# Optimization experiments

Measured on AMD Instinct MI355X. Metric: run time of the kernel, lower is better.

## Reference

```python
import jax, jax.numpy as jnp
import numpy as np

D = 128          # kg_emb_dim
H = 8            # mha_n_heads
N = 20000        # sub-graph nodes per modality
NNZ = 500000     # incidence entries per modality
E = 5000         # hyperedges per modality
C = 50           # context entities
NENT = 50000     # n_entity (rec vocab)


def hyperconv(x, theta, bias, nodes, edges, num_edges):
    # PyG-style HypergraphConv: out = D^-1 H B^-1 H^T (X Theta) + b
    xt = x @ theta                                             # [N, D]
    ones = jnp.ones(nodes.shape[0], xt.dtype)
    e_sum = jax.ops.segment_sum(xt[nodes], edges, num_segments=num_edges)   # [E, D]
    e_deg = jax.ops.segment_sum(ones, edges, num_segments=num_edges)        # [E]
    m = e_sum / jnp.maximum(e_deg, 1.0)[:, None]               # hyperedge means
    n_sum = jax.ops.segment_sum(m[edges], nodes, num_segments=x.shape[0])   # [N, D]
    n_deg = jax.ops.segment_sum(ones, nodes, num_segments=x.shape[0])       # [N]
    return n_sum / jnp.maximum(n_deg, 1.0)[:, None] + bias


def mha(q_x, kv_x, Wq, bq, Wk, bk, Wv, bv, Wo, bo):
    # torch.nn.MultiheadAttention math, batch of 1 (squeezed)
    dh = D // H
    q = (q_x @ Wq + bq).reshape(-1, H, dh)
    k = (kv_x @ Wk + bk).reshape(-1, H, dh)
    v = (kv_x @ Wv + bv).reshape(-1, H, dh)
    scores = jnp.einsum('qhd,khd->hqk', q, k) / jnp.sqrt(jnp.asarray(dh, q.dtype))
    attn = jax.nn.softmax(scores, axis=-1)
    out = jnp.einsum('hqk,khd->qhd', attn, v).reshape(-1, D)
    return out @ Wo + bo


def self_attn(h, a, b):
    # SelfAttentionBatch: softmax(tanh(h a) b) weighted sum over rows
    e = (jnp.tanh(h @ a) @ b)[:, 0]
    return jax.nn.softmax(e) @ h


def setup_inputs() -> dict:
    ks = jax.random.split(jax.random.key(0), 32)
    s = D ** (-0.5)
    inp = {
        'item_emb':   jax.random.normal(ks[0], (N, D), jnp.float32) * s,
        'entity_emb': jax.random.normal(ks[1], (N, D), jnp.float32) * s,
        'word_emb':   jax.random.normal(ks[2], (N, D), jnp.float32) * s,
        'context_entity': jax.random.normal(ks[3], (C, D), jnp.float32) * s,
        'theta_item':   jax.random.normal(ks[4], (D, D), jnp.float32) * s,
        'bias_item':    jax.random.normal(ks[5], (D,), jnp.float32) * 0.02,
        'theta_entity': jax.random.normal(ks[6], (D, D), jnp.float32) * s,
        'bias_entity':  jax.random.normal(ks[7], (D,), jnp.float32) * 0.02,
        'theta_word':   jax.random.normal(ks[8], (D, D), jnp.float32) * s,
        'bias_word':    jax.random.normal(ks[9], (D,), jnp.float32) * 0.02,
        'Wq': jax.random.normal(ks[10], (D, D), jnp.float32) * s,
        'bq': jax.random.normal(ks[11], (D,), jnp.float32) * 0.02,
        'Wk': jax.random.normal(ks[12], (D, D), jnp.float32) * s,
        'bk': jax.random.normal(ks[13], (D,), jnp.float32) * 0.02,
        'Wv': jax.random.normal(ks[14], (D, D), jnp.float32) * s,
        'bv': jax.random.normal(ks[15], (D,), jnp.float32) * 0.02,
        'Wo': jax.random.normal(ks[16], (D, D), jnp.float32) * s,
        'bo': jax.random.normal(ks[17], (D,), jnp.float32) * 0.02,
        'a_his': jax.random.normal(ks[18], (D, D), jnp.float32) * s,
        'b_his': jax.random.normal(ks[19], (D, 1), jnp.float32) * s,
        'a_kg':  jax.random.normal(ks[20], (D, D), jnp.float32) * s,
        'b_kg':  jax.random.normal(ks[21], (D, 1), jnp.float32) * s,
        'rec_W': jax.random.normal(ks[22], (D, NENT), jnp.float32) * s,
        'rec_b': jax.random.normal(ks[23], (NENT,), jnp.float32) * 0.02,
        'item_nodes':   jax.random.randint(ks[24], (NNZ,), 0, N, jnp.int32),
        'item_edges':   jax.random.randint(ks[25], (NNZ,), 0, E, jnp.int32),
        'entity_nodes': jax.random.randint(ks[26], (NNZ,), 0, N, jnp.int32),
        'entity_edges': jax.random.randint(ks[27], (NNZ,), 0, E, jnp.int32),
        'word_nodes':   jax.random.randint(ks[28], (NNZ,), 0, N, jnp.int32),
        'word_edges':   jax.random.randint(ks[29], (NNZ,), 0, E, jnp.int32),
    }
    return inp


def reference(item_emb, entity_emb, word_emb, context_entity,
              theta_item, bias_item, theta_entity, bias_entity, theta_word, bias_word,
              Wq, bq, Wk, bk, Wv, bv, Wo, bo,
              a_his, b_his, a_kg, b_kg, rec_W, rec_b,
              item_nodes, item_edges, entity_nodes, entity_edges, word_nodes, word_edges):
    ih = hyperconv(item_emb, theta_item, bias_item, item_nodes, item_edges, E)
    eh = hyperconv(entity_emb, theta_entity, bias_entity, entity_nodes, entity_edges, E)
    wh = hyperconv(word_emb, theta_word, bias_word, word_nodes, word_edges, E)
    related = jnp.concatenate([ih, eh, wh], axis=0)            # [3N, D]
    # MHItemAttention: context queries attend over related embeddings
    attentive = mha(context_entity, related, Wq, bq, Wk, bk, Wv, bv, Wo, bo)  # [C, D]
    u = self_attn(attentive, a_his, b_his)                     # [D]
    user = jnp.concatenate([context_entity, u[None]], axis=0)  # [C+1, D]
    user_repr = self_attn(user, a_kg, b_kg)                    # [D]
    scores = user_repr @ rec_W + rec_b                         # [NENT]
    return scores
```

## Files before the change

### kernel.cpp

```cpp
#include <hip/hip_runtime.h>
#include <hip/hip_bf16.h>

#define D_ 128
#define H_ 8
#define N_ 20000
#define NNZ_ 500000
#define E_ 5000
#define C_ 50
#define NENT_ 50000
#define NK_ (3*N_)
#define CAPE_ 192
#define CAPN_ 64
#define ENT_PB 4096
#define NBKT 157
#define BCAP 3648
#define ABLK 123
#define NCH3 118
#define KVBLK 235

struct Ptr3f { const float* p[3]; };
struct Ptr3i { const int* p[3]; };
struct GemmB { const float* A[3]; const float* W[3]; unsigned short* C[3]; };

typedef short bf16x8 __attribute__((ext_vector_type(8)));
typedef float f32x4  __attribute__((ext_vector_type(4)));

__device__ __forceinline__ unsigned short f2b(float f){
  unsigned u = __float_as_uint(f);
  u += 0x7FFFu + ((u>>16)&1u);
  return (unsigned short)(u>>16);
}
__device__ __forceinline__ unsigned pk2(float a, float b){
  return (unsigned)f2b(a) | ((unsigned)f2b(b) << 16);
}
__device__ __forceinline__ float blo(unsigned u){ return __uint_as_float(u<<16); }
__device__ __forceinline__ float bhi(unsigned u){ return __uint_as_float(u & 0xFFFF0000u); }

#define PB_PACK 7500
#define PB_Z    7628
#define PB_Q    7629
#define PB_CTX  7693
#define PB_TOT  7743
__global__ __launch_bounds__(256) void prep(Ptr3f xs, unsigned short* __restrict__ xb,
    const float* __restrict__ Wk, const float* __restrict__ Wv, unsigned short* __restrict__ bfB,
    int* __restrict__ gcnt_e, int* __restrict__ gcnt_n,
    const float* __restrict__ ctx, const float* __restrict__ Wq, const float* __restrict__ bq,
    unsigned short* __restrict__ bfQ,
    const float* __restrict__ a2, const float* __restrict__ b2, float* __restrict__ e2)
{
  int bid = blockIdx.x, t = threadIdx.x;
  if (bid < PB_PACK){
    int mod = bid / 2500, blk = bid - mod*2500;
    int i4 = blk*256 + t;
    float4 v = *(const float4*)(xs.p[mod] + (size_t)i4*4);
    ushort4 o; o.x=f2b(v.x); o.y=f2b(v.y); o.z=f2b(v.z); o.w=f2b(v.w);
    *(ushort4*)(xb + (size_t)mod*N_*D_ + (size_t)i4*4) = o;
  } else if (bid < PB_Z){
    int idx = (bid - PB_PACK)*256 + t;
    int j  = idx & 7;
    int L  = (idx >> 3) & 63;
    int kb = (idx >> 9) & 3;
    int tt = idx >> 11;
    int k = kb*32 + (L>>4)*8 + j;
    int x = L & 15;
    float v = (tt < 8) ? Wk[(size_t)k*128 + tt*16 + x] : Wv[(size_t)k*128 + (tt-8)*16 + x];
    bfB[idx] = f2b(v);
  } else if (bid == PB_Z){
    for (int i=t; i<3*NBKT; i+=256){ gcnt_e[i]=0; gcnt_n[i]=0; }
  } else if (bid < PB_CTX){
    int idx = (bid - PB_Q)*256 + t;
    int j  = idx & 7;
    int L  = (idx >> 3) & 63;
    int qt = (idx >> 9) & 3;
    int h  = idx >> 11;
    int k  = ((L>>4)&3)*8 + j;
    int q  = qt*16 + (L & 15);
    float val = 0.f;
    if (k < 16 && q < C_){
      const float* cr = ctx + (size_t)q*128;
      const float* wc = Wq + h*16 + k;
      float s0=0.f,s1=0.f,s2=0.f,s3=0.f;
      for (int d=0; d<128; d+=4){
        s0 = fmaf(cr[d],   wc[(size_t) d   *128], s0);
        s1 = fmaf(cr[d+1], wc[(size_t)(d+1)*128], s1);
        s2 = fmaf(cr[d+2], wc[(size_t)(d+2)*128], s2);
        s3 = fmaf(cr[d+3], wc[(size_t)(d+3)*128], s3);
      }
      val = 0.25f * (s0+s1+s2+s3 + bq[h*16+k]);
    }
    bfQ[idx] = f2b(val);
  } else {
    __shared__ float row[128];
    __shared__ float ps[128][2];
    __shared__ float red[2];
    int q = bid - PB_CTX;
    if (t < 128) row[t] = ctx[(size_t)q*128 + t];
    __syncthreads();
    int c = t & 127, half = t >> 7;
    float s = 0.f;
    int d0 = half*64;
    for (int d=d0; d<d0+64; d+=4){
      s = fmaf(row[d],   a2[(size_t) d   *128 + c], s);
      s = fmaf(row[d+1], a2[(size_t)(d+1)*128 + c], s);
      s = fmaf(row[d+2], a2[(size_t)(d+2)*128 + c], s);
      s = fmaf(row[d+3], a2[(size_t)(d+3)*128 + c], s);
    }
    ps[c][half] = s;
    __syncthreads();
    if (t < 128){
      float v = tanhf(ps[t][0] + ps[t][1]) * b2[t];
      #pragma unroll
      for (int k=32; k>=1; k>>=1) v += __shfl_xor(v, k);
      if ((t & 63) == 0) red[t>>6] = v;
    }
    __syncthreads();
    if (t == 0) e2[q] = red[0] + red[1];
  }
}

__global__ __launch_bounds__(256) void binA(Ptr3i nodes, Ptr3i edges,
    unsigned* __restrict__ pe_part, unsigned* __restrict__ pn_part,
    int* __restrict__ gcnt_e, int* __restrict__ gcnt_n)
{
  __shared__ unsigned lbin[ENT_PB];
  __shared__ int cnt[256], off[256];
  __shared__ int gbase[NBKT];
  __shared__ int wsum[4];
  const int mod = blockIdx.y;
  const int* nd = nodes.p[mod];
  const int* ed = edges.p[mod];
  const int base = blockIdx.x * ENT_PB;
  const int t = threadIdx.x;
  const int lane = t & 63, w = t >> 6;

  int myn[16], mye[16], pos[16];
  #pragma unroll
  for (int k=0;k<16;k++){
    int i = base + t + k*256;
    if (i < NNZ_){ myn[k]=nd[i]; mye[k]=ed[i]; }
    else { myn[k]=-1; mye[k]=-1; }
  }

  cnt[t] = 0;
  __syncthreads();
  #pragma unroll
  for (int k=0;k<16;k++)
    if (mye[k] >= 0) pos[k] = atomicAdd(&cnt[mye[k]>>5], 1);
  __syncthreads();
  {
    int v = cnt[t], s = v;
    #pragma unroll
    for (int d=1; d<64; d<<=1){ int u=__shfl_up(s,d); if (lane>=d) s+=u; }
    if (lane==63) wsum[w]=s;
    __syncthreads();
    int wb=0;
    for (int i=0;i<w;i++) wb+=wsum[i];
    off[t] = wb + s - v;
    __syncthreads();
  }
  #pragma unroll
  for (int k=0;k<16;k++)
    if (mye[k] >= 0)
      lbin[off[mye[k]>>5] + pos[k]] = ((unsigned)mye[k] << 15) | (unsigned)myn[k];
  if (t < NBKT && cnt[t] > 0) gbase[t] = atomicAdd(&gcnt_e[mod*NBKT + t], cnt[t]);
  __syncthreads();
  {
    int total = off[255];
    unsigned* dstreg = pe_part + (size_t)mod*NBKT*BCAP;
    for (int i=t; i<total; i+=256){
      unsigned pk = lbin[i];
      int b = pk >> 20;
      int gp = gbase[b] + (i - off[b]);
      if (gp < BCAP) dstreg[(size_t)b*BCAP + gp] = pk;
    }
  }
  __syncthreads();

  cnt[t] = 0;
  __syncthreads();
  #pragma unroll
  for (int k=0;k<16;k++)
    if (myn[k] >= 0) pos[k] = atomicAdd(&cnt[myn[k]>>7], 1);
  __syncthreads();
  {
    int v = cnt[t], s = v;
    #pragma unroll
    for (int d=1; d<64; d<<=1){ int u=__shfl_up(s,d); if (lane>=d) s+=u; }
    if (lane==63) wsum[w]=s;
    __syncthreads();
    int wb=0;
    for (int i=0;i<w;i++) wb+=wsum[i];
    off[t] = wb + s - v;
    __syncthreads();
  }
  #pragma unroll
  for (int k=0;k<16;k++)
    if (myn[k] >= 0)
      lbin[off[myn[k]>>7] + pos[k]] = ((unsigned)myn[k] << 13) | (unsigned)mye[k];
  if (t < NBKT && cnt[t] > 0) gbase[t] = atomicAdd(&gcnt_n[mod*NBKT + t], cnt[t]);
  __syncthreads();
  {
    int total = off[255];
    unsigned* dstreg = pn_part + (size_t)mod*NBKT*BCAP;
    for (int i=t; i<total; i+=256){
      unsigned pk = lbin[i];
      int b = pk >> 20;
      int gp = gbase[b] + (i - off[b]);
      if (gp < BCAP) dstreg[(size_t)b*BCAP + gp] = pk;
    }
  }
}

__global__ __launch_bounds__(256) void binB(const unsigned* __restrict__ pe_part,
    const unsigned* __restrict__ pn_part,
    const int* __restrict__ gcnt_e, const int* __restrict__ gcnt_n,
    int* __restrict__ cnt_all, int* __restrict__ cntA_e,
    unsigned short* __restrict__ e_slot, unsigned short* __restrict__ n_slot)
{
  __shared__ unsigned short ls[128*CAPN_];
  __shared__ int lc[128];
  const int y = blockIdx.y, b = blockIdx.x, t = threadIdx.x;
  if (y < 3){
    const int mod = y;
    if (t < 64) lc[t] = 0;
    __syncthreads();
    int cnt = gcnt_e[mod*NBKT + b];
    if (cnt > BCAP) cnt = BCAP;
    const unsigned* src = pe_part + ((size_t)mod*NBKT + b)*BCAP;
    for (int i=t; i<cnt; i+=256){
      unsigned pk = src[i];
      int el = (pk >> 15) - b*32;
      int n  = pk & 0x7FFF;
      if (n < (N_>>1)){
        int p = atomicAdd(&lc[el], 1);
        if (p < 96) ls[el*CAPE_ + p] = (unsigned short)n;
      } else {
        int p = atomicAdd(&lc[32 + el], 1);
        if (p < 96) ls[el*CAPE_ + (CAPE_-1 - p)] = (unsigned short)n;
      }
    }
    __syncthreads();
    int rows = E_ - b*32; if (rows > 32) rows = 32;
    if (t < rows){
      cnt_all[mod*(E_+N_) + b*32 + t] = lc[t] + lc[32+t];
      cntA_e[mod*E_ + b*32 + t] = lc[t];
    }
    const unsigned* lsu = (const unsigned*)ls;
    unsigned* dst = (unsigned*)(e_slot + ((size_t)mod*E_ + b*32)*CAPE_);
    int tot = rows*CAPE_/2;
    for (int i=t; i<tot; i+=256) dst[i] = lsu[i];
  } else {
    const int mod = y - 3;
    if (t < 128) lc[t] = 0;
    __syncthreads();
    int cnt = gcnt_n[mod*NBKT + b];
    if (cnt > BCAP) cnt = BCAP;
    const unsigned* src = pn_part + ((size_t)mod*NBKT + b)*BCAP;
    for (int i=t; i<cnt; i+=256){
      unsigned pk = src[i];
      int nl = (pk >> 13) - b*128;
      int e  = pk & 0x1FFF;
      int p = atomicAdd(&lc[nl], 1);
      if (p < CAPN_) ls[nl*CAPN_ + p] = (unsigned short)e;
    }
    __syncthreads();
    int rows = N_ - b*128; if (rows > 128) rows = 128;
    if (t < rows) cnt_all[mod*(E_+N_) + E_ + b*128 + t] = lc[t];
    const unsigned* lsu = (const unsigned*)ls;
    unsigned* dst = (unsigned*)(n_slot + ((size_t)mod*N_ + b*128)*CAPN_);
    int tot = rows*CAPN_/2;
    for (int i=t; i<tot; i+=256) dst[i] = lsu[i];
  }
}

#define EGB 3752
template<int PHASE>
__global__ __launch_bounds__(256) void e_gather_ph(const unsigned short* __restrict__ xb,
    const int* __restrict__ cnt_all, const int* __restrict__ cntA_e,
    const unsigned short* __restrict__ e_slot, float* __restrict__ m_mean)
{
  const int bid = blockIdx.x;
  const int x = bid & 7, k = bid >> 3;
  int mod, r;
  if (x < 6){
    mod = x / 3;
    int li = x - mod*3;
    int c = 417 - (li == 2);
    if (k < c){
      r = k*3 + li;
    } else {
      int hg = 52*x + (x >= 3) + (k - c);
      mod = 2; r = 938 + hg;
      if (r >= E_/4) return;
    }
  } else {
    mod = 2; r = k*2 + (x - 6);
  }
  const int w = threadIdx.x >> 6, lane = threadIdx.x & 63;
  const int rgrp = lane >> 4, dl = lane & 15;
  const int e = r*4 + w;
  const unsigned short* xt = xb + (size_t)mod*N_*D_;
  int cnt = cnt_all[mod*(E_+N_) + e];
  int cAr = cntA_e[mod*E_ + e];
  int cA = (cAr < 96) ? cAr : 96;
  int cBr = cnt - cAr;
  int cB = (cBr < 96) ? cBr : 96;
  const unsigned short* slot = e_slot + ((size_t)mod*E_ + e)*CAPE_;
  float a0=0.f,a1=0.f,a2=0.f,a3=0.f,a4=0.f,a5=0.f,a6=0.f,a7=0.f;

  if (PHASE == 0){
    int sv0 = slot[lane], sv1 = slot[64 + lane];
    for (int j=0; j<cA; j+=32){
      uint4 uu[8];
      #pragma unroll
      for (int kk=0;kk<8;kk++){
        int jr = j + 4*kk + rgrp;
        int jj = (jr < cA) ? jr : 0;
        int i0 = __shfl(sv0, jj & 63);
        int i1 = __shfl(sv1, jj & 63);
        int idx = (jj < 64) ? i0 : i1;
        uu[kk] = *(const uint4*)(xt + (size_t)idx*128 + dl*8);
      }
      #pragma unroll
      for (int kk=0;kk<8;kk++){
        int jr = j + 4*kk + rgrp;
        bool v = jr < cA;
        unsigned x0 = v ? uu[kk].x : 0u, x1 = v ? uu[kk].y : 0u;
        unsigned x2 = v ? uu[kk].z : 0u, x3 = v ? uu[kk].w : 0u;
        a0 += blo(x0); a1 += bhi(x0); a2 += blo(x1); a3 += bhi(x1);
        a4 += blo(x2); a5 += bhi(x2); a6 += blo(x3); a7 += bhi(x3);
      }
    }
  } else {
    int sv1 = slot[64 + lane], sv2 = slot[128 + lane];
    int s0 = CAPE_ - cB;
    for (int j=0; j<cB; j+=32){
      uint4 uu[8];
      #pragma unroll
      for (int kk=0;kk<8;kk++){
        int jr = j + 4*kk + rgrp;
        int jj = (jr < cB) ? (s0 + jr) : (CAPE_-1);
        int i1 = __shfl(sv1, jj & 63);
        int i2 = __shfl(sv2, jj & 63);
        int idx = (jj < 128) ? i1 : i2;
        uu[kk] = *(const uint4*)(xt + (size_t)idx*128 + dl*8);
      }
      #pragma unroll
      for (int kk=0;kk<8;kk++){
        int jr = j + 4*kk + rgrp;
        bool v = jr < cB;
        unsigned x0 = v ? uu[kk].x : 0u, x1 = v ? uu[kk].y : 0u;
        unsigned x2 = v ? uu[kk].z : 0u, x3 = v ? uu[kk].w : 0u;
        a0 += blo(x0); a1 += bhi(x0); a2 += blo(x1); a3 += bhi(x1);
        a4 += blo(x2); a5 += bhi(x2); a6 += blo(x3); a7 += bhi(x3);
      }
    }
  }

  #pragma unroll
  for (int s=16; s<=32; s<<=1){
    a0 += __shfl_xor(a0, s); a1 += __shfl_xor(a1, s);
    a2 += __shfl_xor(a2, s); a3 += __shfl_xor(a3, s);
    a4 += __shfl_xor(a4, s); a5 += __shfl_xor(a5, s);
    a6 += __shfl_xor(a6, s); a7 += __shfl_xor(a7, s);
  }
  if (rgrp == 0){
    float* dst = m_mean + ((size_t)mod*E_ + e)*128 + dl*8;
    if (PHASE == 0){
      float4 o1; o1.x=a0; o1.y=a1; o1.z=a2; o1.w=a3;
      float4 o2; o2.x=a4; o2.y=a5; o2.z=a6; o2.w=a7;
      *(float4*)dst = o1;
      *(float4*)(dst + 4) = o2;
    } else {
      float inv = 1.f / fmaxf((float)cnt, 1.f);
      float4 o1 = *(const float4*)dst;
      float4 o2 = *(const float4*)(dst + 4);
      o1.x = (o1.x + a0)*inv; o1.y = (o1.y + a1)*inv;
      o1.z = (o1.z + a2)*inv; o1.w = (o1.w + a3)*inv;
      o2.x = (o2.x + a4)*inv; o2.y = (o2.y + a5)*inv;
      o2.z = (o2.z + a6)*inv; o2.w = (o2.w + a7)*inv;
      *(float4*)dst = o1;
      *(float4*)(dst + 4) = o2;
    }
  }
}

__global__ __launch_bounds__(256) void gemm_b(GemmB g, int M)
{
  const float* A = g.A[blockIdx.y];
  const float* W = g.W[blockIdx.y];
  unsigned short* Cout = g.C[blockIdx.y];
  __shared__ float As[64][33];
  __shared__ float Ws[32][128];
  const int t  = threadIdx.x;
  const int br = blockIdx.x * 64;
  const int r0 = (t >> 5) * 8;
  const int c0 = (t & 31) * 4;
  const int lr = t >> 2;
  const int lk = (t & 3) * 8;
  const int wk = t >> 5;

  float acc[8][4];
  #pragma unroll
  for (int i=0;i<8;i++){ acc[i][0]=0.f; acc[i][1]=0.f; acc[i][2]=0.f; acc[i][3]=0.f; }

  for (int kb=0; kb<128; kb+=32){
    float av[8];
    const int grow = br + lr;
    if (grow < M){
      const float* p = A + (size_t)grow*128 + kb + lk;
      float4 a = ((const float4*)p)[0], b = ((const float4*)p)[1];
      av[0]=a.x;av[1]=a.y;av[2]=a.z;av[3]=a.w;av[4]=b.x;av[5]=b.y;av[6]=b.z;av[7]=b.w;
    } else {
      #pragma unroll
      for (int j=0;j<8;j++) av[j]=0.f;
    }
    float4 wv4[4];
    #pragma unroll
    for (int kk=0;kk<4;kk++) wv4[kk] = *(const float4*)&W[(size_t)(kb + wk + kk*8)*128 + c0];

    __syncthreads();
    #pragma unroll
    for (int j=0;j<8;j++) As[lr][lk+j] = av[j];
    #pragma unroll
    for (int kk=0;kk<4;kk++) *(float4*)&Ws[wk + kk*8][c0] = wv4[kk];
    __syncthreads();

    #pragma unroll
    for (int k=0;k<32;k++){
      float4 wv = *(const float4*)&Ws[k][c0];
      #pragma unroll
      for (int i=0;i<8;i++){
        float a = As[r0+i][k];
        acc[i][0] = fmaf(a, wv.x, acc[i][0]);
        acc[i][1] = fmaf(a, wv.y, acc[i][1]);
        acc[i][2] = fmaf(a, wv.z, acc[i][2]);
        acc[i][3] = fmaf(a, wv.w, acc[i][3]);
      }
    }
  }

  #pragma unroll
  for (int i=0;i<8;i++){
    int gr = br + r0 + i;
    if (gr < M){
      ushort4 o;
      o.x=f2b(acc[i][0]); o.y=f2b(acc[i][1]); o.z=f2b(acc[i][2]); o.w=f2b(acc[i][3]);
      *(ushort4*)(Cout + (size_t)gr*128 + c0) = o;
    }
  }
}

__global__ __launch_bounds__(256) void n_gather_w(const unsigned short* __restrict__ m_buf,
    const int* __restrict__ cnt_all, const unsigned short* __restrict__ n_slot,
    Ptr3f biases, unsigned short* __restrict__ relbf)
{
  int mod = blockIdx.y;
  int w = threadIdx.x >> 6, lane = threadIdx.x & 63;
  int rgrp = lane >> 4, dl = lane & 15;
  int n = blockIdx.x*4 + w;
  const unsigned short* m = m_buf + (size_t)mod*E_*D_;
  int cnt = cnt_all[mod*(E_+N_) + E_ + n];
  int c2 = (cnt < CAPN_) ? cnt : CAPN_;
  const unsigned short* slot = n_slot + ((size_t)mod*N_ + n)*CAPN_;
  int sv = slot[lane];
  float a0=0.f,a1=0.f,a2=0.f,a3=0.f,a4=0.f,a5=0.f,a6=0.f,a7=0.f;
  for (int j=0; j<c2; j+=32){
    uint4 uu[8];
    #pragma unroll
    for (int k=0;k<8;k++){
      int jr = j + 4*k + rgrp;
      int jj = (jr < c2) ? jr : 0;
      int idx = __shfl(sv, jj);
      uu[k] = *(const uint4*)(m + (size_t)idx*128 + dl*8);
    }
    #pragma unroll
    for (int k=0;k<8;k++){
      int jr = j + 4*k + rgrp;
      bool v = jr < c2;
      unsigned x0 = v ? uu[k].x : 0u, x1 = v ? uu[k].y : 0u;
      unsigned x2 = v ? uu[k].z : 0u, x3 = v ? uu[k].w : 0u;
      a0 += blo(x0); a1 += bhi(x0); a2 += blo(x1); a3 += bhi(x1);
      a4 += blo(x2); a5 += bhi(x2); a6 += blo(x3); a7 += bhi(x3);
    }
  }
  #pragma unroll
  for (int s=16; s<=32; s<<=1){
    a0 += __shfl_xor(a0, s); a1 += __shfl_xor(a1, s);
    a2 += __shfl_xor(a2, s); a3 += __shfl_xor(a3, s);
    a4 += __shfl_xor(a4, s); a5 += __shfl_xor(a5, s);
    a6 += __shfl_xor(a6, s); a7 += __shfl_xor(a7, s);
  }
  if (rgrp == 0){
    float inv = 1.f / fmaxf((float)cnt, 1.f);
    const float* bs = biases.p[mod] + dl*8;
    uint4 o;
    o.x = pk2(a0*inv + bs[0], a1*inv + bs[1]);
    o.y = pk2(a2*inv + bs[2], a3*inv + bs[3]);
    o.z = pk2(a4*inv + bs[4], a5*inv + bs[5]);
    o.w = pk2(a6*inv + bs[6], a7*inv + bs[7]);
    *(uint4*)(relbf + ((size_t)mod*N_ + n)*128 + dl*8) = o;
  }
}

__global__ __launch_bounds__(256) void gemm_kv_mfma(const unsigned short* __restrict__ relbf,
    const unsigned short* __restrict__ bfB, const float* __restrict__ bk,
    const float* __restrict__ bv, unsigned short* __restrict__ Kb,
    unsigned short* __restrict__ Vtg)
{
  __shared__ unsigned short Bs[32768];
  const int t = threadIdx.x, w = t >> 6, L = t & 63;
  const int m = L & 15, quad = L >> 4, x = m;

  {
    const uint4* src = (const uint4*)bfB;
    uint4* dst = (uint4*)Bs;
    for (int i = t; i < 4096; i += 256) dst[i] = src[i];
  }
  __syncthreads();

  const int rowbase = blockIdx.x*256;
  for (int g = 0; g < 4; g++){
    const int j0 = rowbase + g*64 + w*16;

    bf16x8 a[4];
    {
      int row = j0 + m;
      int rowc = (row < NK_) ? row : (NK_-1);
      #pragma unroll
      for (int kb=0; kb<4; kb++)
        a[kb] = *(const bf16x8*)(relbf + (size_t)rowc*128 + kb*32 + quad*8);
    }

    f32x4 acc[16];
    #pragma unroll
    for (int tt=0; tt<16; tt++) acc[tt] = (f32x4){0.f,0.f,0.f,0.f};

    #pragma unroll
    for (int kb=0; kb<4; kb++){
      #pragma unroll
      for (int tt=0; tt<16; tt++){
        bf16x8 b = *(const bf16x8*)&Bs[(((tt*4 + kb)*64 + L) << 3)];
        acc[tt] = __builtin_amdgcn_mfma_f32_16x16x32_bf16(a[kb], b, acc[tt], 0, 0, 0);
      }
    }

    #pragma unroll
    for (int tt=0; tt<16; tt++){
      int h = tt & 7, kv = tt >> 3;
      float bias = (kv ? bv : bk)[h*16 + x];
      #pragma unroll
      for (int r=0; r<4; r++){
        int jr = j0 + quad*4 + r;
        if (jr < NK_){
          unsigned short val = f2b(acc[tt][r] + bias);
          if (kv == 0) Kb[(((size_t)h*NK_ + jr) << 4) + x] = val;
          else         Vtg[((size_t)(h*16 + x))*NK_ + jr] = val;
        }
      }
    }
  }
}

__global__ __launch_bounds__(256) void flash3(const unsigned short* __restrict__ Kb,
    const unsigned short* __restrict__ Vtg, const unsigned short* __restrict__ bfQ,
    float* __restrict__ part)
{
  __shared__ unsigned short P_lds[4][64][40];
  __shared__ float mbuf[4][64][18];
  const int c = blockIdx.x, h = blockIdx.y;
  const int t = threadIdx.x, w = t >> 6, L = t & 63;
  const int n = L & 15, quad = L >> 4;

  bf16x8 qb[4];
  #pragma unroll
  for (int qt=0; qt<4; qt++)
    qb[qt] = *(const bf16x8*)(bfQ + (((h*4 + qt)*64 + L) << 3));

  float Mc[4], Lc[4];
  f32x4 accq[4];
  #pragma unroll
  for (int qt=0; qt<4; qt++){ Mc[qt] = -INFINITY; Lc[qt] = 0.f; accq[qt] = (f32x4){0.f,0.f,0.f,0.f}; }

  const int base = c*512 + w*128;
  unsigned* Pw = (unsigned*)&P_lds[w][0][0];

  for (int tile=0; tile<4; tile++){
    const int j0 = base + tile*32;
    const bool dead = (j0 >= NK_);

    bf16x8 a0 = (bf16x8){0,0,0,0,0,0,0,0};
    bf16x8 a1 = a0;
    if (quad < 2){
      int k0 = j0 + n;      if (k0 > NK_-1) k0 = NK_-1;
      int k1 = j0 + 16 + n; if (k1 > NK_-1) k1 = NK_-1;
      a0 = *(const bf16x8*)(Kb + (((size_t)h*NK_ + k0) << 4) + quad*8);
      a1 = *(const bf16x8*)(Kb + (((size_t)h*NK_ + k1) << 4) + quad*8);
    }
    f32x4 s0[4], s1[4];
    #pragma unroll
    for (int qt=0; qt<4; qt++){
      s0[qt] = __builtin_amdgcn_mfma_f32_16x16x32_bf16(a0, qb[qt], (f32x4){0.f,0.f,0.f,0.f}, 0,0,0);
      s1[qt] = __builtin_amdgcn_mfma_f32_16x16x32_bf16(a1, qb[qt], (f32x4){0.f,0.f,0.f,0.f}, 0,0,0);
    }

    #pragma unroll
    for (int qt=0; qt<4; qt++){
      float mt = s0[qt][0];
      mt = fmaxf(mt, s0[qt][1]); mt = fmaxf(mt, s0[qt][2]); mt = fmaxf(mt, s0[qt][3]);
      mt = fmaxf(mt, s1[qt][0]); mt = fmaxf(mt, s1[qt][1]);
      mt = fmaxf(mt, s1[qt][2]); mt = fmaxf(mt, s1[qt][3]);
      mt = fmaxf(mt, __shfl_xor(mt, 16));
      mt = fmaxf(mt, __shfl_xor(mt, 32));
      float Mn = fmaxf(Mc[qt], mt);
      float corr = __expf(Mc[qt] - Mn);
      Mc[qt] = Mn;
      float p0[4], p1[4];
      #pragma unroll
      for (int r=0;r<4;r++){
        p0[r] = __expf(s0[qt][r] - Mn);
        p1[r] = __expf(s1[qt][r] - Mn);
      }
      if (dead){
        #pragma unroll
        for (int r=0;r<4;r++){ p0[r]=0.f; p1[r]=0.f; }
      }
      float lt = p0[0]+p0[1]+p0[2]+p0[3]+p1[0]+p1[1]+p1[2]+p1[3];
      lt += __shfl_xor(lt, 16);
      lt += __shfl_xor(lt, 32);
      Lc[qt] = Lc[qt]*corr + lt;
      int rb = (qt*16 + n)*20;
      Pw[rb + quad*2]     = pk2(p0[0], p0[1]);
      Pw[rb + quad*2 + 1] = pk2(p0[2], p0[3]);
      Pw[rb + 8 + quad*2]     = pk2(p1[0], p1[1]);
      Pw[rb + 8 + quad*2 + 1] = pk2(p1[2], p1[3]);
      #pragma unroll
      for (int r=0;r<4;r++){
        float cr = __shfl(corr, quad*4 + r);
        accq[qt][r] *= cr;
      }
    }
    __syncthreads();

    bf16x8 bv_;
    {
      int va = j0 + quad*8; if (va > NK_-8) va = NK_-8;
      bv_ = *(const bf16x8*)(Vtg + ((size_t)(h*16 + n))*NK_ + va);
    }
    #pragma unroll
    for (int qt=0; qt<4; qt++){
      bf16x8 pa = *(const bf16x8*)&P_lds[w][qt*16 + n][quad*8];
      accq[qt] = __builtin_amdgcn_mfma_f32_16x16x32_bf16(pa, bv_, accq[qt], 0,0,0);
    }
    __syncthreads();
  }

  #pragma unroll
  for (int qt=0; qt<4; qt++){
    #pragma unroll
    for (int r=0; r<4; r++)
      mbuf[w][qt*16 + quad*4 + r][2 + n] = accq[qt][r];
    if (quad == 0){
      mbuf[w][qt*16 + n][0] = Mc[qt];
      mbuf[w][qt*16 + n][1] = Lc[qt];
    }
  }
  __syncthreads();
  if (t < C_){
    float M = mbuf[0][t][0], Lm = mbuf[0][t][1];
    float A[16];
    #pragma unroll
    for (int i=0;i<16;i++) A[i] = mbuf[0][t][2+i];
    #pragma unroll
    for (int ww=1; ww<4; ww++){
      float pm = mbuf[ww][t][0], pl = mbuf[ww][t][1];
      if (pl > 0.f){
        float mn = fmaxf(M, pm);
        float c1 = __expf(M - mn), c2 = __expf(pm - mn);
        Lm = Lm*c1 + pl*c2;
        #pragma unroll
        for (int i=0;i<16;i++) A[i] = A[i]*c1 + mbuf[ww][t][2+i]*c2;
        M = mn;
      }
    }
    float* pp = part + ((size_t)(h*NCH3 + c)*C_ + t)*18;
    pp[0] = M; pp[1] = Lm;
    #pragma unroll
    for (int i=0;i<16;i++) pp[2+i] = A[i];
  }
}

__global__ __launch_bounds__(512) void merge_oproj_e1(const float* __restrict__ part,
    const float* __restrict__ Wo, const float* __restrict__ bo,
    const float* __restrict__ a1, const float* __restrict__ b1,
    float* __restrict__ attentive, float* __restrict__ e1)
{
  __shared__ float row[128];
  __shared__ float ps[128][4];
  __shared__ float orow[128];
  __shared__ float red[2];
  const int q = blockIdx.x, t = threadIdx.x;
  const int h = t >> 6, lane = t & 63;

  {
    float M = -1e30f, L = 0.f;
    float A[16];
    #pragma unroll
    for (int i=0;i<16;i++) A[i] = 0.f;

    #pragma unroll
    for (int cc=0; cc<2; cc++){
      int c = lane + cc*64;
      if (c < NCH3){
        const float* p = part + ((size_t)(h*NCH3 + c)*C_ + q)*18;
        float pm = p[0], pl = p[1];
        if (pl > 0.f){
          float Mn = fmaxf(M, pm);
          float w1 = __expf(M - Mn), w2 = __expf(pm - Mn);
          L = L*w1 + pl*w2;
          #pragma unroll
          for (int i=0;i<16;i++) A[i] = fmaf(A[i], w1, p[2+i]*w2);
          M = Mn;
        }
      }
    }
    #pragma unroll
    for (int d=32; d>=1; d>>=1){
      float pm = __shfl_xor(M, d);
      float pl = __shfl_xor(L, d);
      float Ao[16];
      #pragma unroll
      for (int i=0;i<16;i++) Ao[i] = __shfl_xor(A[i], d);
      float Mn = fmaxf(M, pm);
      float w1 = __expf(M - Mn), w2 = __expf(pm - Mn);
      L = L*w1 + pl*w2;
      #pragma unroll
      for (int i=0;i<16;i++) A[i] = fmaf(A[i], w1, Ao[i]*w2);
      M = Mn;
    }
    if (lane == 0){
      float invL = 1.f / L;
      #pragma unroll
      for (int i=0;i<16;i++) row[h*16 + i] = A[i]*invL;
    }
  }
  __syncthreads();

  const int c = t & 127, seg = t >> 7;
  {
    float s = 0.f;
    int d0 = seg*32;
    for (int d=d0; d<d0+32; d+=4){
      s = fmaf(row[d],   Wo[(size_t) d   *128 + c], s);
      s = fmaf(row[d+1], Wo[(size_t)(d+1)*128 + c], s);
      s = fmaf(row[d+2], Wo[(size_t)(d+2)*128 + c], s);
      s = fmaf(row[d+3], Wo[(size_t)(d+3)*128 + c], s);
    }
    ps[c][seg] = s;
  }
  __syncthreads();
  if (t < 128){
    float o = ps[t][0]+ps[t][1]+ps[t][2]+ps[t][3] + bo[t];
    attentive[(size_t)q*128 + t] = o;
    orow[t] = o;
  }
  __syncthreads();
  {
    float s = 0.f;
    int d0 = seg*32;
    for (int d=d0; d<d0+32; d+=4){
      s = fmaf(orow[d],   a1[(size_t) d   *128 + c], s);
      s = fmaf(orow[d+1], a1[(size_t)(d+1)*128 + c], s);
      s = fmaf(orow[d+2], a1[(size_t)(d+2)*128 + c], s);
      s = fmaf(orow[d+3], a1[(size_t)(d+3)*128 + c], s);
    }
    ps[c][seg] = s;
  }
  __syncthreads();
  if (t < 128){
    float v = tanhf(ps[t][0]+ps[t][1]+ps[t][2]+ps[t][3]) * b1[t];
    #pragma unroll
    for (int k=32; k>=1; k>>=1) v += __shfl_xor(v, k);
    if ((t & 63) == 0) red[t>>6] = v;
  }
  __syncthreads();
  if (t == 0) e1[q] = red[0] + red[1];
}

__global__ __launch_bounds__(128) void tail_mid(const float* __restrict__ attentive,
    const float* __restrict__ ctx, const float* __restrict__ a2, const float* __restrict__ b2,
    const float* __restrict__ e1, const float* __restrict__ e2, float* __restrict__ user_repr)
{
  __shared__ float p[64];
  __shared__ float u[128];
  __shared__ float red[2];
  __shared__ float p2[64];
  const int t = threadIdx.x;

  if (t == 0){
    float mx=-INFINITY;
    for (int i=0;i<C_;i++) mx=fmaxf(mx,e1[i]);
    float ss=0.f;
    for (int i=0;i<C_;i++){ p[i]=__expf(e1[i]-mx); ss+=p[i]; }
    float inv=1.f/ss;
    for (int i=0;i<C_;i++) p[i]*=inv;
  }
  __syncthreads();
  {
    float s=0.f;
    for (int r=0;r<C_;r++) s = fmaf(p[r], attentive[(size_t)r*128 + t], s);
    u[t] = s;
  }
  __syncthreads();
  {
    float s0=0.f,s1=0.f,s2=0.f,s3=0.f;
    for (int d=0; d<128; d+=4){
      s0 = fmaf(u[d],   a2[(size_t) d   *128 + t], s0);
      s1 = fmaf(u[d+1], a2[(size_t)(d+1)*128 + t], s1);
      s2 = fmaf(u[d+2], a2[(size_t)(d+2)*128 + t], s2);
      s3 = fmaf(u[d+3], a2[(size_t)(d+3)*128 + t], s3);
    }
    float v = tanhf(s0+s1+s2+s3) * b2[t];
    #pragma unroll
    for (int k=32; k>=1; k>>=1) v += __shfl_xor(v, k);
    if ((t & 63) == 0) red[t>>6] = v;
  }
  __syncthreads();
  if (t == 0){
    float elast = red[0] + red[1];
    float mx=elast;
    for (int i=0;i<C_;i++) mx=fmaxf(mx,e2[i]);
    float ss=0.f;
    for (int i=0;i<C_;i++){ p2[i]=__expf(e2[i]-mx); ss+=p2[i]; }
    float pl = __expf(elast-mx); ss += pl;
    float inv=1.f/ss;
    for (int i=0;i<C_;i++) p2[i]*=inv;
    p2[C_] = pl*inv;
  }
  __syncthreads();
  {
    float s=0.f;
    for (int r=0;r<C_;r++) s = fmaf(p2[r], ctx[(size_t)r*128 + t], s);
    s = fmaf(p2[C_], u[t], s);
    user_repr[t] = s;
  }
}

__global__ __launch_bounds__(256) void scores_k(const float* __restrict__ ur,
    const float* __restrict__ recW, const float* __restrict__ recb, float* __restrict__ out)
{
  __shared__ float u[128];
  int t = threadIdx.x;
  if (t < 128) u[t] = ur[t];
  __syncthreads();
  int j = blockIdx.x*256 + t;
  if (j < NENT_){
    float s0=0.f,s1=0.f,s2=0.f,s3=0.f;
    for (int d=0; d<128; d+=4){
      s0 = fmaf(u[d],   recW[(size_t) d   *NENT_ + j], s0);
      s1 = fmaf(u[d+1], recW[(size_t)(d+1)*NENT_ + j], s1);
      s2 = fmaf(u[d+2], recW[(size_t)(d+2)*NENT_ + j], s2);
      s3 = fmaf(u[d+3], recW[(size_t)(d+3)*NENT_ + j], s3);
    }
    out[j] = s0+s1+s2+s3 + recb[j];
  }
}

extern "C" void kernel_launch(void* const* d_in, const int* in_sizes, int n_in,
                              void* d_out, int out_size, void* d_ws, size_t ws_size,
                              hipStream_t stream)
{
  auto f32 = [&](int i){ return (const float*)d_in[i]; };
  Ptr3i nodes = {{(const int*)d_in[24], (const int*)d_in[26], (const int*)d_in[28]}};
  Ptr3i edges = {{(const int*)d_in[25], (const int*)d_in[27], (const int*)d_in[29]}};

  char* base = (char*)d_ws;
  int*   cnt_all = (int*)base;
  int*   gcnt_e  = (int*)(base + 300064);
  int*   gcnt_n  = gcnt_e + NBKT*3;
  unsigned short* n_slot = (unsigned short*)(base + 300064 + 4096);
  float* m_mean  = (float*)((char*)n_slot + 7680000);
  unsigned short* m_buf = (unsigned short*)((char*)m_mean + 7680000);
  unsigned short* relbf = (unsigned short*)((char*)m_buf + 3840000);
  unsigned short* bfB   = (unsigned short*)((char*)relbf + 15360000);
  unsigned short* bfQ   = (unsigned short*)((char*)bfB + 65536);
  float* attentive = (float*)((char*)bfQ + 32768);
  float* user_repr = (float*)((char*)attentive + 25600);
  float* e1buf     = user_repr + 128;
  float* e2buf     = e1buf + 64;
  int*   cntA_e    = (int*)(e2buf + 64);
  float* fpart = (float*)relbf;
  char* U = (char*)(cntA_e + 3*E_);
  unsigned* pe_part = (unsigned*)U;
  unsigned* pn_part = pe_part + (size_t)3*NBKT*BCAP;
  unsigned short* e_slot = (unsigned short*)(pn_part + (size_t)3*NBKT*BCAP);
  unsigned short* xb     = e_slot + (size_t)3*E_*CAPE_;
  unsigned short* Kb  = (unsigned short*)U;
  unsigned short* Vtg = Kb + (size_t)H_*NK_*16;

  Ptr3f xs = {{f32(0), f32(1), f32(2)}};
  prep<<<PB_TOT, 256, 0, stream>>>(xs, xb, f32(12), f32(14), bfB, gcnt_e, gcnt_n,
                                   f32(3), f32(10), f32(11), bfQ, f32(20), f32(21), e2buf);

  binA<<<dim3(ABLK, 3), 256, 0, stream>>>(nodes, edges, pe_part, pn_part, gcnt_e, gcnt_n);
  binB<<<dim3(NBKT, 6), 256, 0, stream>>>(pe_part, pn_part, gcnt_e, gcnt_n, cnt_all, cntA_e,
                                          e_slot, n_slot);

  e_gather_ph<0><<<EGB, 256, 0, stream>>>(xb, cnt_all, cntA_e, e_slot, m_mean);
  e_gather_ph<1><<<EGB, 256, 0, stream>>>(xb, cnt_all, cntA_e, e_slot, m_mean);
  GemmB g;
  for (int mod=0; mod<3; mod++){
    g.A[mod] = m_mean + (size_t)mod*E_*D_;
    g.W[mod] = f32(4 + 2*mod);
    g.C[mod] = m_buf + (size_t)mod*E_*D_;
  }
  gemm_b<<<dim3((E_+63)/64, 3), 256, 0, stream>>>(g, E_);
  Ptr3f biases = {{f32(5), f32(7), f32(9)}};
  n_gather_w<<<dim3(N_/4, 3), 256, 0, stream>>>(m_buf, cnt_all, n_slot, biases, relbf);

  gemm_kv_mfma<<<KVBLK, 256, 0, stream>>>(relbf, bfB, f32(13), f32(15), Kb, Vtg);
  flash3<<<dim3(NCH3, H_), 256, 0, stream>>>(Kb, Vtg, bfQ, fpart);
  merge_oproj_e1<<<C_, 512, 0, stream>>>(fpart, f32(16), f32(17), f32(18), f32(19),
                                         attentive, e1buf);

  tail_mid<<<1, 128, 0, stream>>>(attentive, f32(3), f32(20), f32(21), e1buf, e2buf, user_repr);
  scores_k<<<(NENT_+255)/256, 256, 0, stream>>>(user_repr, f32(22), f32(23), (float*)d_out);
}
```

Measured before the change: 348.4 us.

## Pad gather slots with zero-row sentinels to drop per-element bounds masking

Slot tables in shared memory are pre-filled with the index of a dedicated all-zero row appended after the bf16 feature and hyperedge-mean buffers, and prep zeroes those rows. The gather loops can then run to a multiple of 32 with no per-element validity selects or clamped indices, and accumulation uses packed two-wide float vectors. This removes compare/select instructions from the hot gather loops, at the cost of extra shared-memory fill work in binB, a shifted workspace layout, and wasted loads of the zero row in padded tails.

```diff
diff --git a/kernel.cpp b/kernel.cpp
--- a/kernel.cpp
+++ b/kernel.cpp
@@ -24,6 +24,7 @@
 
 typedef short bf16x8 __attribute__((ext_vector_type(8)));
 typedef float f32x4  __attribute__((ext_vector_type(4)));
+typedef float f32x2  __attribute__((ext_vector_type(2)));
 
 __device__ __forceinline__ unsigned short f2b(float f){
   unsigned u = __float_as_uint(f);
@@ -35,6 +36,21 @@
 }
 __device__ __forceinline__ float blo(unsigned u){ return __uint_as_float(u<<16); }
 __device__ __forceinline__ float bhi(unsigned u){ return __uint_as_float(u & 0xFFFF0000u); }
+
+#define GBATCH(SRC, SREG, LBASE) { \
+  uint4 uu[8]; \
+  _Pragma("unroll") \
+  for (int kk=0;kk<8;kk++){ \
+    int idx = __shfl(SREG, (LBASE) + 4*kk + rgrp); \
+    uu[kk] = *(const uint4*)((SRC) + (size_t)idx*128 + dl*8); \
+  } \
+  _Pragma("unroll") \
+  for (int kk=0;kk<8;kk++){ \
+    a01 += (f32x2){blo(uu[kk].x), bhi(uu[kk].x)}; \
+    a23 += (f32x2){blo(uu[kk].y), bhi(uu[kk].y)}; \
+    a45 += (f32x2){blo(uu[kk].z), bhi(uu[kk].z)}; \
+    a67 += (f32x2){blo(uu[kk].w), bhi(uu[kk].w)}; \
+  } }
 
 #define PB_PACK 7500
 #define PB_Z    7628
@@ -43,7 +59,7 @@
 #define PB_TOT  7743
 __global__ __launch_bounds__(256) void prep(Ptr3f xs, unsigned short* __restrict__ xb,
     const float* __restrict__ Wk, const float* __restrict__ Wv, unsigned short* __restrict__ bfB,
-    int* __restrict__ gcnt_e, int* __restrict__ gcnt_n,
+    int* __restrict__ gcnt_e, int* __restrict__ gcnt_n, unsigned short* __restrict__ mzero,
     const float* __restrict__ ctx, const float* __restrict__ Wq, const float* __restrict__ bq,
     unsigned short* __restrict__ bfQ,
     const float* __restrict__ a2, const float* __restrict__ b2, float* __restrict__ e2)
@@ -67,6 +83,8 @@
     bfB[idx] = f2b(v);
   } else if (bid == PB_Z){
     for (int i=t; i<3*NBKT; i+=256){ gcnt_e[i]=0; gcnt_n[i]=0; }
+    if (t < 64)       ((unsigned*)(xb    + (size_t)60000*128))[t]    = 0u;
+    else if (t < 128) ((unsigned*)(mzero + (size_t)15000*128))[t-64] = 0u;
   } else if (bid < PB_CTX){
     int idx = (bid - PB_Q)*256 + t;
     int j  = idx & 7;
@@ -222,6 +240,12 @@
   const int y = blockIdx.y, b = blockIdx.x, t = threadIdx.x;
   if (y < 3){
     const int mod = y;
+    {
+      unsigned short dmy = (unsigned short)(60000 - mod*20000);
+      unsigned dd = (unsigned)dmy * 0x10001u;
+      unsigned* lsu32 = (unsigned*)ls;
+      for (int i=t; i<32*CAPE_/2; i+=256) lsu32[i] = dd;
+    }
     if (t < 64) lc[t] = 0;
     __syncthreads();
     int cnt = gcnt_e[mod*NBKT + b];
@@ -251,6 +275,12 @@
     for (int i=t; i<tot; i+=256) dst[i] = lsu[i];
   } else {
     const int mod = y - 3;
+    {
+      unsigned short dmy = (unsigned short)(15000 - mod*5000);
+      unsigned dd = (unsigned)dmy * 0x10001u;
+      unsigned* lsu32 = (unsigned*)ls;
+      for (int i=t; i<128*CAPN_/2; i+=256) lsu32[i] = dd;
+    }
     if (t < 128) lc[t] = 0;
     __syncthreads();
     int cnt = gcnt_n[mod*NBKT + b];
@@ -306,57 +336,26 @@
   int cBr = cnt - cAr;
   int cB = (cBr < 96) ? cBr : 96;
   const unsigned short* slot = e_slot + ((size_t)mod*E_ + e)*CAPE_;
-  float a0=0.f,a1=0.f,a2=0.f,a3=0.f,a4=0.f,a5=0.f,a6=0.f,a7=0.f;
+  f32x2 a01={0.f,0.f}, a23={0.f,0.f}, a45={0.f,0.f}, a67={0.f,0.f};
 
   if (PHASE == 0){
     int sv0 = slot[lane], sv1 = slot[64 + lane];
-    for (int j=0; j<cA; j+=32){
-      uint4 uu[8];
-      #pragma unroll
-      for (int kk=0;kk<8;kk++){
-        int jr = j + 4*kk + rgrp;
-        int jj = (jr < cA) ? jr : 0;
-        int i0 = __shfl(sv0, jj & 63);
-        int i1 = __shfl(sv1, jj & 63);
-        int idx = (jj < 64) ? i0 : i1;
-        uu[kk] = *(const uint4*)(xt + (size_t)idx*128 + dl*8);
-      }
-      #pragma unroll
-      for (int kk=0;kk<8;kk++){
-        int jr = j + 4*kk + rgrp;
-        bool v = jr < cA;
-        unsigned x0 = v ? uu[kk].x : 0u, x1 = v ? uu[kk].y : 0u;
-        unsigned x2 = v ? uu[kk].z : 0u, x3 = v ? uu[kk].w : 0u;
-        a0 += blo(x0); a1 += bhi(x0); a2 += blo(x1); a3 += bhi(x1);
-        a4 += blo(x2); a5 += bhi(x2); a6 += blo(x3); a7 += bhi(x3);
-      }
-    }
+    int cA32 = (cA + 31) & ~31;
+    int j = 0;
+    int lim0 = (cA32 < 64) ? cA32 : 64;
+    for (; j < lim0; j += 32) GBATCH(xt, sv0, j);
+    for (; j < cA32; j += 32) GBATCH(xt, sv1, j - 64);
   } else {
     int sv1 = slot[64 + lane], sv2 = slot[128 + lane];
-    int s0 = CAPE_ - cB;
-    for (int j=0; j<cB; j+=32){
-      uint4 uu[8];
-      #pragma unroll
-      for (int kk=0;kk<8;kk++){
-        int jr = j + 4*kk + rgrp;
-        int jj = (jr < cB) ? (s0 + jr) : (CAPE_-1);
-        int i1 = __shfl(sv1, jj & 63);
-        int i2 = __shfl(sv2, jj & 63);
-        int idx = (jj < 128) ? i1 : i2;
-        uu[kk] = *(const uint4*)(xt + (size_t)idx*128 + dl*8);
-      }
-      #pragma unroll
-      for (int kk=0;kk<8;kk++){
-        int jr = j + 4*kk + rgrp;
-        bool v = jr < cB;
-        unsigned x0 = v ? uu[kk].x : 0u, x1 = v ? uu[kk].y : 0u;
-        unsigned x2 = v ? uu[kk].z : 0u, x3 = v ? uu[kk].w : 0u;
-        a0 += blo(x0); a1 += bhi(x0); a2 += blo(x1); a3 += bhi(x1);
-        a4 += blo(x2); a5 += bhi(x2); a6 += blo(x3); a7 += bhi(x3);
-      }
-    }
-  }
-
+    int cB32 = (cB + 31) & ~31;
+    int s0 = CAPE_ - cB32;
+    for (int j = s0; j < CAPE_; j += 32){
+      if (j < 128) GBATCH(xt, sv1, j - 64)
+      else         GBATCH(xt, sv2, j - 128)
+    }
+  }
+
+  float a0=a01.x, a1=a01.y, a2=a23.x, a3=a23.y, a4=a45.x, a5=a45.y, a6=a67.x, a7=a67.y;
   #pragma unroll
   for (int s=16; s<=32; s<<=1){
     a0 += __shfl_xor(a0, s); a1 += __shfl_xor(a1, s);
@@ -462,28 +461,13 @@
   const unsigned short* m = m_buf + (size_t)mod*E_*D_;
   int cnt = cnt_all[mod*(E_+N_) + E_ + n];
   int c2 = (cnt < CAPN_) ? cnt : CAPN_;
+  int c2p = (c2 + 31) & ~31;
   const unsigned short* slot = n_slot + ((size_t)mod*N_ + n)*CAPN_;
   int sv = slot[lane];
-  float a0=0.f,a1=0.f,a2=0.f,a3=0.f,a4=0.f,a5=0.f,a6=0.f,a7=0.f;
-  for (int j=0; j<c2; j+=32){
-    uint4 uu[8];
-    #pragma unroll
-    for (int k=0;k<8;k++){
-      int jr = j + 4*k + rgrp;
-      int jj = (jr < c2) ? jr : 0;
-      int idx = __shfl(sv, jj);
-      uu[k] = *(const uint4*)(m + (size_t)idx*128 + dl*8);
-    }
-    #pragma unroll
-    for (int k=0;k<8;k++){
-      int jr = j + 4*k + rgrp;
-      bool v = jr < c2;
-      unsigned x0 = v ? uu[k].x : 0u, x1 = v ? uu[k].y : 0u;
-      unsigned x2 = v ? uu[k].z : 0u, x3 = v ? uu[k].w : 0u;
-      a0 += blo(x0); a1 += bhi(x0); a2 += blo(x1); a3 += bhi(x1);
-      a4 += blo(x2); a5 += bhi(x2); a6 += blo(x3); a7 += bhi(x3);
-    }
-  }
+  f32x2 a01={0.f,0.f}, a23={0.f,0.f}, a45={0.f,0.f}, a67={0.f,0.f};
+  for (int j=0; j<c2p; j+=32) GBATCH(m, sv, j);
+
+  float a0=a01.x, a1=a01.y, a2=a23.x, a3=a23.y, a4=a45.x, a5=a45.y, a6=a67.x, a7=a67.y;
   #pragma unroll
   for (int s=16; s<=32; s<<=1){
     a0 += __shfl_xor(a0, s); a1 += __shfl_xor(a1, s);
@@ -881,7 +865,7 @@
   unsigned short* n_slot = (unsigned short*)(base + 300064 + 4096);
   float* m_mean  = (float*)((char*)n_slot + 7680000);
   unsigned short* m_buf = (unsigned short*)((char*)m_mean + 7680000);
-  unsigned short* relbf = (unsigned short*)((char*)m_buf + 3840000);
+  unsigned short* relbf = (unsigned short*)((char*)m_buf + 3840256);
   unsigned short* bfB   = (unsigned short*)((char*)relbf + 15360000);
   unsigned short* bfQ   = (unsigned short*)((char*)bfB + 65536);
   float* attentive = (float*)((char*)bfQ + 32768);
@@ -899,7 +883,7 @@
   unsigned short* Vtg = Kb + (size_t)H_*NK_*16;
 
   Ptr3f xs = {{f32(0), f32(1), f32(2)}};
-  prep<<<PB_TOT, 256, 0, stream>>>(xs, xb, f32(12), f32(14), bfB, gcnt_e, gcnt_n,
+  prep<<<PB_TOT, 256, 0, stream>>>(xs, xb, f32(12), f32(14), bfB, gcnt_e, gcnt_n, m_buf,
                                    f32(3), f32(10), f32(11), bfQ, f32(20), f32(21), e2buf);
 
   binA<<<dim3(ABLK, 3), 256, 0, stream>>>(nodes, edges, pe_part, pn_part, gcnt_e, gcnt_n);
```

Result: faster. 336.1 us (-3.5%).
